# Kernel tuning notes

Measured on AMD Instinct MI355X. Metric: run time of the kernel, lower is better.

Reference implementation:

```python
import jax, jax.numpy as jnp
import numpy as np

B, HGT, WID, D, NS = 4, 64, 128, 128, 2
LN_EPS = 1e-5

def layer_norm(x, g, b):
    m = jnp.mean(x, axis=-1, keepdims=True)
    v = jnp.mean((x - m) ** 2, axis=-1, keepdims=True)
    return (x - m) * jax.lax.rsqrt(v + LN_EPS) * g + b

def setup_inputs() -> dict:
    key = jax.random.key(0)
    ks = jax.random.split(key, 8)
    src = jax.random.normal(ks[0], (B, HGT * WID, D), jnp.float32)
    L = (HGT // NS) * (WID // NS)  # 2048
    s = 0.05
    return {
        "source": src,
        "target": src,  # identical -> self-attention branch in original
        "shifted_window_attn_mask": jax.random.normal(ks[1], (NS * NS, L, L), jnp.float32),
        "shifted_window_attn_mask_1d": jnp.zeros((NS, WID // NS, WID // NS), jnp.float32),
        "height": HGT,
        "width": WID,
        "attn_num_splits": NS,
        "with_shift": 1,
        "Wq": jax.random.normal(ks[2], (D, D), jnp.float32) * s,
        "Wk": jax.random.normal(ks[3], (D, D), jnp.float32) * s,
        "Wv": jax.random.normal(ks[4], (D, D), jnp.float32) * s,
        "Wm": jax.random.normal(ks[5], (D, D), jnp.float32) * s,
        "g1": jnp.ones((D,), jnp.float32),
        "b1": jnp.zeros((D,), jnp.float32),
        "W1": jax.random.normal(ks[6], (2 * D, 8 * D), jnp.float32) * s,
        "W2": jax.random.normal(ks[7], (8 * D, D), jnp.float32) * s,
        "g2": jnp.ones((D,), jnp.float32),
        "b2": jnp.zeros((D,), jnp.float32),
    }

def _shifted_window_self_attn(q, k, v, ns, with_shift, h, w, attn_mask):
    b, _, c = q.shape
    hh, ww = h // ns, w // ns  # window sizes
    sh, sw = hh // 2, ww // 2
    L = hh * ww

    def to_windows(x):
        x = x.reshape(b, h, w, c)
        if with_shift:
            x = jnp.roll(x, shift=(-sh, -sw), axis=(1, 2))
        # (b, ns, hh, ns, ww, c) -> (b*ns*ns, hh*ww, c)
        x = x.reshape(b, ns, hh, ns, ww, c).transpose(0, 1, 3, 2, 4, 5)
        return x.reshape(b * ns * ns, L, c)

    qw, kw, vw = to_windows(q), to_windows(k), to_windows(v)
    scores = jnp.einsum("bqc,bkc->bqk", qw, kw) / (c ** 0.5)  # (b*ns^2, L, L)
    if with_shift:
        scores = (scores.reshape(b, ns * ns, L, L) + attn_mask).reshape(b * ns * ns, L, L)
    attn = jax.nn.softmax(scores, axis=-1)
    out = jnp.einsum("bqk,bkc->bqc", attn, vw)
    # merge windows back
    out = out.reshape(b, ns, ns, hh, ww, c).transpose(0, 1, 3, 2, 4, 5).reshape(b, h, w, c)
    if with_shift:
        out = jnp.roll(out, shift=(sh, sw), axis=(1, 2))
    return out.reshape(b, h * w, c)

def reference(source, target, shifted_window_attn_mask, shifted_window_attn_mask_1d,
              height, width, attn_num_splits, with_shift,
              Wq, Wk, Wv, Wm, g1, b1, W1, W2, g2, b2):
    # target == source -> self-attention, attn_num_splits > 1 -> shifted-window path
    q = source @ Wq
    k = target @ Wk
    v = target @ Wv
    message = _shifted_window_self_attn(q, k, v, attn_num_splits, with_shift,
                                        height, width, shifted_window_attn_mask)
    message = layer_norm(message @ Wm, g1, b1)
    h = jnp.concatenate([source, message], axis=-1)  # (B, HW, 2D)
    message = jax.nn.gelu(h @ W1, approximate=False) @ W2
    message = layer_norm(message, g2, b2)
    return source + message
```

## Files before the change

kernel.cpp:

```cpp
#include <hip/hip_runtime.h>

typedef unsigned short u16;
typedef __bf16 bf16x8 __attribute__((ext_vector_type(8)));
typedef float f32x4 __attribute__((ext_vector_type(4)));

#define MFMA(a, b, c) __builtin_amdgcn_mfma_f32_16x16x32_bf16(a, b, c, 0, 0, 0)


__device__ __forceinline__ u16 f2b(float f) {
  unsigned u = __builtin_bit_cast(unsigned, f);
  u += 0x7fffu + ((u >> 16) & 1u);
  return (u16)(u >> 16);
}
__device__ __forceinline__ float b2f(u16 h) {
  unsigned u = (unsigned)h << 16;
  return __builtin_bit_cast(float, u);
}
__device__ __forceinline__ void glds16(const u16* g, u16* l) {
  __builtin_amdgcn_global_load_lds((const __attribute__((address_space(1))) void*)g,
                                   (__attribute__((address_space(3))) void*)l, 16, 0, 0);
}

#define QW_OFF   ((size_t)0)
#define KW_OFF   ((size_t)8 << 20)
#define VBUF_OFF ((size_t)16 << 20)
#define O1_OFF   ((size_t)24 << 20)
#define O2_OFF   ((size_t)40 << 20)
#define SRCB_OFF ((size_t)64 << 20)
#define MSG1_OFF ((size_t)72 << 20)
#define L1_OFF   ((size_t)80 << 20)
#define L2P_OFF  (((size_t)80 << 20) + 131072)
#define WQT_OFF  (((size_t)80 << 20) + 262144)
#define WKT_OFF  (WQT_OFF + 32768)
#define WVT_OFF  (WQT_OFF + 65536)
#define WMT_OFF  (WQT_OFF + 98304)
#define W1T_OFF  (WQT_OFF + 131072)
#define W2T_OFF  (WQT_OFF + 655360)

__global__ void k_prep(const float* __restrict__ wq, const float* __restrict__ wk,
                       const float* __restrict__ wv, const float* __restrict__ wm,
                       const float* __restrict__ w1, const float* __restrict__ w2,
                       u16* __restrict__ wqt, u16* __restrict__ wkt,
                       u16* __restrict__ wvt, u16* __restrict__ wmt,
                       u16* __restrict__ w1t, u16* __restrict__ w2t) {
  int t = blockIdx.x * 256 + threadIdx.x;
  if (t < 65536) {
    int m = t >> 14, loc = t & 16383;
    int n = loc >> 7, k = loc & 127;
    const float* s = (m == 0) ? wq : (m == 1) ? wk : (m == 2) ? wv : wm;
    u16* d = (m == 0) ? wqt : (m == 1) ? wkt : (m == 2) ? wvt : wmt;
    const float sc = (m == 0) ? 0.08838834764831845f : 1.0f;
    d[n * 128 + k] = f2b(s[k * 128 + n] * sc);
  } else if (t < 65536 + 262144) {
    int loc = t - 65536;
    int n = loc >> 8, k = loc & 255;
    w1t[n * 256 + k] = f2b(w1[k * 1024 + n]);
  } else if (t < 65536 + 262144 + 131072) {
    int loc = t - 327680;
    int n = loc >> 10, k = loc & 1023;
    w2t[n * 1024 + k] = f2b(w2[k * 128 + n]);
  }
}

__global__ __launch_bounds__(256, 2)
void k_qkv(const float* __restrict__ src,
           const u16* __restrict__ wtq, const u16* __restrict__ wtk,
           const u16* __restrict__ wtv,
           u16* __restrict__ qw, u16* __restrict__ kw, u16* __restrict__ vbuf,
           u16* __restrict__ srcb) {
  __shared__ __align__(16) u16 At[64 * 136];
  __shared__ __align__(16) u16 Bt[128 * 136];
  const int tid = threadIdx.x, bid = blockIdx.x;
  const int lane = tid & 63, wid = tid >> 6;
  const int l15 = lane & 15, quad = lane >> 4;

  {
    const int row = tid >> 2, part = tid & 3;
    const int t = bid * 64 + row;
    const int g = t >> 11, p = t & 2047;
    const int b = g >> 2, wi = (g >> 1) & 1, wj = g & 1;
    const int ii = p >> 6, jj = p & 63;
    const int y = (wi * 32 + ii + 16) & 63;
    const int x = (wj * 64 + jj + 32) & 127;
    const int srow = b * 8192 + y * 128 + x;
    const float4* sp = (const float4*)(src + srow * 128) + part * 8;
    u16* lp = &At[row * 136 + part * 32];
    u16* gp = srcb + srow * 128 + part * 32;
#pragma unroll
    for (int q = 0; q < 8; ++q) {
      float4 v = sp[q];
      ushort4 h = make_ushort4(f2b(v.x), f2b(v.y), f2b(v.z), f2b(v.w));
      *(ushort4*)(lp + q * 4) = h;
      *(ushort4*)(gp + q * 4) = h;
    }
  }
  __syncthreads();

  bf16x8 afrag[4];
  const int arow = wid * 16 + l15;
#pragma unroll
  for (int kk = 0; kk < 4; ++kk)
    afrag[kk] = *(const bf16x8*)&At[arow * 136 + kk * 32 + quad * 8];

  const f32x4 fz = {0.f, 0.f, 0.f, 0.f};
#pragma unroll 1
  for (int m = 0; m < 3; ++m) {
    const u16* wp = (m == 0) ? wtq : (m == 1) ? wtk : wtv;
    {
      const int n = tid >> 1, half = tid & 1;
      const uint4* sp = (const uint4*)(wp + n * 128 + half * 64);
      uint4* dp = (uint4*)&Bt[n * 136 + half * 64];
#pragma unroll
      for (int q = 0; q < 8; ++q) dp[q] = sp[q];
    }
    __syncthreads();
    f32x4 acc[8];
#pragma unroll
    for (int nt = 0; nt < 8; ++nt) acc[nt] = fz;
#pragma unroll
    for (int kk = 0; kk < 4; ++kk) {
#pragma unroll
      for (int nt = 0; nt < 8; ++nt) {
        bf16x8 bfr = *(const bf16x8*)&Bt[(nt * 16 + l15) * 136 + kk * 32 + quad * 8];
        acc[nt] = MFMA(afrag[kk], bfr, acc[nt]);
      }
    }
    const int t0 = bid * 64 + wid * 16 + quad * 4;
    if (m < 2) {
      u16* dst = (m == 0) ? qw : kw;
#pragma unroll
      for (int nt = 0; nt < 8; ++nt) {
        const int d = nt * 16 + l15;
#pragma unroll
        for (int r = 0; r < 4; ++r) dst[(t0 + r) * 128 + d] = f2b(acc[nt][r]);
      }
    } else {
      const int g = bid >> 5;
      const int p0 = t0 & 2047;
#pragma unroll
      for (int nt = 0; nt < 8; ++nt) {
        const int d = nt * 16 + l15;
        ushort4 hv = make_ushort4(f2b(acc[nt][0]), f2b(acc[nt][1]),
                                  f2b(acc[nt][2]), f2b(acc[nt][3]));
        *(ushort4*)&vbuf[g * 262144 + d * 2048 + p0] = hv;
      }
    }
    __syncthreads();
  }
}

__global__ __launch_bounds__(256, 2)
void k_attn(const u16* __restrict__ qw, const u16* __restrict__ kw,
            const u16* __restrict__ vbuf, const float* __restrict__ mask,
            u16* __restrict__ o1, u16* __restrict__ o2,
            float* __restrict__ l1, float* __restrict__ l2) {
  __shared__ __align__(16) u16 Kt[2][64 * 128];
  __shared__ __align__(16) u16 Pt[128 * 40];
  const int tid = threadIdx.x;
  const int bid = (blockIdx.x & 7) * 64 + (blockIdx.x >> 3);
  const int lane = tid & 63, wid = tid >> 6;
  const int l15 = lane & 15, quad = lane >> 4;
  const int qb = bid & 15, half = (bid >> 4) & 1, g = bid >> 5;
  const int w = g & 3;
  const int k0 = half * 1024;
  const u16* kbase = kw + g * 262144 + k0 * 128;
  const u16* vbase = vbuf + g * 262144 + k0;
  const int qrow0 = qb * 128 + wid * 32;
  const float* mlane = mask + (size_t)w * 4194304 + (size_t)(qrow0 + quad * 4) * 2048 + k0 + l15;

  int offk[4], dstb[4];
#pragma unroll
  for (int j = 0; j < 4; ++j) {
    const int s = wid * 256 + j * 64 + lane;
    const int rk = s >> 4, bk = (s & 15) ^ (rk & 15);
    offk[j] = rk * 128 + bk * 8;
    dstb[j] = (wid * 256 + j * 64) * 8;
  }

  bf16x8 qfrag[2][4];
#pragma unroll
  for (int qs = 0; qs < 2; ++qs) {
    const u16* qp = qw + g * 262144 + (qrow0 + qs * 16 + l15) * 128 + quad * 8;
#pragma unroll
    for (int kk = 0; kk < 4; ++kk) qfrag[qs][kk] = *(const bf16x8*)(qp + kk * 32);
  }
  const f32x4 fz = {0.f, 0.f, 0.f, 0.f};
  f32x4 o[2][8];
#pragma unroll
  for (int qs = 0; qs < 2; ++qs)
#pragma unroll
    for (int nt = 0; nt < 8; ++nt) o[qs][nt] = fz;
  float lr[2][4] = {{0.f, 0.f, 0.f, 0.f}, {0.f, 0.f, 0.f, 0.f}};
  const float L2E = 1.4426950408889634f;

#pragma unroll
  for (int j = 0; j < 4; ++j) glds16(kbase + offk[j], &Kt[0][dstb[j]]);
  float mpf[16];
#pragma unroll
  for (int qs = 0; qs < 2; ++qs)
#pragma unroll
    for (int ntl = 0; ntl < 2; ++ntl)
#pragma unroll
      for (int r = 0; r < 4; ++r)
        mpf[qs * 8 + ntl * 4 + r] = mlane[(qs * 16 + r) * 2048 + ntl * 16];

#pragma unroll 1
  for (int kt = 0; kt < 16; ++kt) {
    const int p = kt & 1;
    __syncthreads();
    if (kt < 15) {
      const u16* kb = kbase + (kt + 1) * 8192;
#pragma unroll
      for (int j = 0; j < 4; ++j) glds16(kb + offk[j], &Kt[p ^ 1][dstb[j]]);
    }
#pragma unroll
    for (int ks = 0; ks < 2; ++ks) {
      bf16x8 vf[8];
      const u16* vp = vbase + kt * 64 + ks * 32 + quad * 8;
#pragma unroll
      for (int nt = 0; nt < 8; ++nt)
        vf[nt] = *(const bf16x8*)(vp + (size_t)(nt * 16 + l15) * 2048);
      float mn[16];
      const bool hasn = (kt < 15) || (ks == 0);
      const int ncol = kt * 64 + 32 + ks * 32;
      if (hasn) {
#pragma unroll
        for (int qs = 0; qs < 2; ++qs)
#pragma unroll
          for (int ntl = 0; ntl < 2; ++ntl)
#pragma unroll
            for (int r = 0; r < 4; ++r)
              mn[qs * 8 + ntl * 4 + r] = mlane[(qs * 16 + r) * 2048 + ncol + ntl * 16];
      }
      f32x4 s[2][2];
#pragma unroll
      for (int qs = 0; qs < 2; ++qs)
#pragma unroll
        for (int ntl = 0; ntl < 2; ++ntl)
#pragma unroll
          for (int r = 0; r < 4; ++r) s[qs][ntl][r] = mpf[qs * 8 + ntl * 4 + r];
#pragma unroll
      for (int kk = 0; kk < 4; ++kk)
#pragma unroll
        for (int ntl = 0; ntl < 2; ++ntl) {
          bf16x8 kfr = *(const bf16x8*)&Kt[p][(ks * 32 + ntl * 16 + l15) * 128 +
                                             (((kk * 4 + quad) ^ l15) * 8)];
          s[0][ntl] = MFMA(qfrag[0][kk], kfr, s[0][ntl]);
          s[1][ntl] = MFMA(qfrag[1][kk], kfr, s[1][ntl]);
        }
#pragma unroll
      for (int qs = 0; qs < 2; ++qs)
#pragma unroll
        for (int ntl = 0; ntl < 2; ++ntl)
#pragma unroll
          for (int r = 0; r < 4; ++r) {
            const float pv = exp2f(s[qs][ntl][r] * L2E);
            lr[qs][r] += pv;
            Pt[(wid * 32 + qs * 16 + quad * 4 + r) * 40 + ntl * 16 + l15] = f2b(pv);
          }
      bf16x8 pf0 = *(const bf16x8*)&Pt[(wid * 32 + l15) * 40 + quad * 8];
      bf16x8 pf1 = *(const bf16x8*)&Pt[(wid * 32 + 16 + l15) * 40 + quad * 8];
#pragma unroll
      for (int nt = 0; nt < 8; ++nt) {
        o[0][nt] = MFMA(pf0, vf[nt], o[0][nt]);
        o[1][nt] = MFMA(pf1, vf[nt], o[1][nt]);
      }
      if (hasn) {
#pragma unroll
        for (int i = 0; i < 16; ++i) mpf[i] = mn[i];
      }
    }
  }

#pragma unroll
  for (int off = 1; off < 16; off <<= 1)
#pragma unroll
    for (int qs = 0; qs < 2; ++qs)
#pragma unroll
      for (int r = 0; r < 4; ++r) lr[qs][r] += __shfl_xor(lr[qs][r], off, 16);
  u16* op = half ? o2 : o1;
  float* lp = half ? l2 : l1;
#pragma unroll
  for (int qs = 0; qs < 2; ++qs) {
    const int t0 = g * 2048 + qrow0 + qs * 16 + quad * 4;
#pragma unroll
    for (int r = 0; r < 4; ++r) {
      const float inv = 1.f / lr[qs][r];
#pragma unroll
      for (int nt = 0; nt < 8; ++nt)
        op[(size_t)(t0 + r) * 128 + nt * 16 + l15] = f2b(o[qs][nt][r] * inv);
      if (l15 == 0) lp[t0 + r] = lr[qs][r];
    }
  }
}

__global__ __launch_bounds__(256, 2)
void k_wmln(const u16* __restrict__ o1, const u16* __restrict__ o2,
            const float* __restrict__ l1, const float* __restrict__ l2,
            const u16* __restrict__ wmt, const float* __restrict__ g1,
            const float* __restrict__ b1, u16* __restrict__ msg1) {
  __shared__ __align__(16) u16 At[64 * 136];
  __shared__ __align__(16) u16 Bt[128 * 136];
  const int tid = threadIdx.x, bid = blockIdx.x;
  const int lane = tid & 63, wid = tid >> 6;
  const int l15 = lane & 15, quad = lane >> 4;
  {
    const int row = tid >> 2, part = tid & 3;
    const int m = bid * 64 + row;
    const float la = l1[m], lb = l2[m];
    const float wA = la / (la + lb), wB = lb / (la + lb);
    const u16* p1 = o1 + (size_t)m * 128 + part * 32;
    const u16* p2 = o2 + (size_t)m * 128 + part * 32;
    u16* lp = &At[row * 136 + part * 32];
#pragma unroll
    for (int q = 0; q < 4; ++q) {
      ushort4 xa = *(const ushort4*)(p1 + q * 8);
      ushort4 xb = *(const ushort4*)(p1 + q * 8 + 4);
      ushort4 ya = *(const ushort4*)(p2 + q * 8);
      ushort4 yb = *(const ushort4*)(p2 + q * 8 + 4);
      ushort4 ha = make_ushort4(f2b(b2f(xa.x) * wA + b2f(ya.x) * wB),
                                f2b(b2f(xa.y) * wA + b2f(ya.y) * wB),
                                f2b(b2f(xa.z) * wA + b2f(ya.z) * wB),
                                f2b(b2f(xa.w) * wA + b2f(ya.w) * wB));
      ushort4 hb = make_ushort4(f2b(b2f(xb.x) * wA + b2f(yb.x) * wB),
                                f2b(b2f(xb.y) * wA + b2f(yb.y) * wB),
                                f2b(b2f(xb.z) * wA + b2f(yb.z) * wB),
                                f2b(b2f(xb.w) * wA + b2f(yb.w) * wB));
      *(ushort4*)(lp + q * 8) = ha;
      *(ushort4*)(lp + q * 8 + 4) = hb;
    }
  }
  {
    const int n = tid >> 1, half = tid & 1;
    const uint4* sp = (const uint4*)(wmt + n * 128 + half * 64);
    uint4* dp = (uint4*)&Bt[n * 136 + half * 64];
#pragma unroll
    for (int q = 0; q < 8; ++q) dp[q] = sp[q];
  }
  __syncthreads();
  bf16x8 afrag[4];
  const int arow = wid * 16 + l15;
#pragma unroll
  for (int kk = 0; kk < 4; ++kk)
    afrag[kk] = *(const bf16x8*)&At[arow * 136 + kk * 32 + quad * 8];
  const f32x4 fz = {0.f, 0.f, 0.f, 0.f};
  f32x4 acc[8];
#pragma unroll
  for (int nt = 0; nt < 8; ++nt) acc[nt] = fz;
#pragma unroll
  for (int kk = 0; kk < 4; ++kk)
#pragma unroll
    for (int nt = 0; nt < 8; ++nt) {
      bf16x8 bfr = *(const bf16x8*)&Bt[(nt * 16 + l15) * 136 + kk * 32 + quad * 8];
      acc[nt] = MFMA(afrag[kk], bfr, acc[nt]);
    }
  float sum[4] = {0, 0, 0, 0}, sq[4] = {0, 0, 0, 0};
#pragma unroll
  for (int nt = 0; nt < 8; ++nt)
#pragma unroll
    for (int r = 0; r < 4; ++r) {
      const float v = acc[nt][r];
      sum[r] += v;
      sq[r] += v * v;
    }
#pragma unroll
  for (int off = 1; off < 16; off <<= 1)
#pragma unroll
    for (int r = 0; r < 4; ++r) {
      sum[r] += __shfl_xor(sum[r], off, 16);
      sq[r] += __shfl_xor(sq[r], off, 16);
    }
  float mean[4], rstd[4];
#pragma unroll
  for (int r = 0; r < 4; ++r) {
    mean[r] = sum[r] * (1.f / 128.f);
    const float var = sq[r] * (1.f / 128.f) - mean[r] * mean[r];
    rstd[r] = rsqrtf(var + 1e-5f);
  }
  const int t0 = bid * 64 + wid * 16 + quad * 4;
#pragma unroll
  for (int nt = 0; nt < 8; ++nt) {
    const int d = nt * 16 + l15;
    const float gg = g1[d], bb = b1[d];
#pragma unroll
    for (int r = 0; r < 4; ++r) {
      const int tt = t0 + r;
      const int gw = tt >> 11, pp = tt & 2047;
      const int bb2 = gw >> 2, wi = (gw >> 1) & 1, wj = gw & 1;
      const int ii = pp >> 6, jj = pp & 63;
      const int yy = (wi * 32 + ii + 16) & 63;
      const int xx = (wj * 64 + jj + 32) & 127;
      msg1[(bb2 * 8192 + yy * 128 + xx) * 128 + d] =
          f2b((acc[nt][r] - mean[r]) * rstd[r] * gg + bb);
    }
  }
}

__global__ __launch_bounds__(256, 2)
void k_mlp(const u16* __restrict__ srcb, const u16* __restrict__ msg1,
           const u16* __restrict__ w1t, const u16* __restrict__ w2t,
           const float* __restrict__ g2, const float* __restrict__ b2,
           const float* __restrict__ src, float* __restrict__ out) {
  __shared__ __align__(16) u16 Bt1[64 * 256];
  __shared__ __align__(16) u16 Bt2[128 * 64];
  __shared__ __align__(16) u16 Ht[64 * 72];
  const int tid = threadIdx.x, bid = blockIdx.x;
  const int lane = tid & 63, wid = tid >> 6;
  const int l15 = lane & 15, quad = lane >> 4;

  int off1[8], db1[8], off2[4], db2[4];
#pragma unroll
  for (int j = 0; j < 8; ++j) {
    const int s = wid * 512 + j * 64 + lane;
    const int r = s >> 5, c = s & 31;
    off1[j] = r * 256 + (c ^ (r & 15)) * 8;
    db1[j] = (wid * 512 + j * 64) * 8;
  }
#pragma unroll
  for (int j = 0; j < 4; ++j) {
    const int s = wid * 256 + j * 64 + lane;
    const int r = s >> 3, c = s & 7;
    off2[j] = r * 1024 + (c ^ (r & 7)) * 8;
    db2[j] = (wid * 256 + j * 64) * 8;
  }

  bf16x8 afrag[8];
  {
    const int row = bid * 64 + wid * 16 + l15;
    const u16* sp = srcb + (size_t)row * 128 + quad * 8;
    const u16* mp = msg1 + (size_t)row * 128 + quad * 8;
#pragma unroll
    for (int kk = 0; kk < 4; ++kk) {
      afrag[kk] = *(const bf16x8*)(sp + kk * 32);
      afrag[kk + 4] = *(const bf16x8*)(mp + kk * 32);
    }
  }
  const f32x4 fz = {0.f, 0.f, 0.f, 0.f};
  f32x4 oacc[8];
#pragma unroll
  for (int nt = 0; nt < 8; ++nt) oacc[nt] = fz;

#pragma unroll 1
  for (int hc = 0; hc < 16; ++hc) {
    __syncthreads();
#pragma unroll
    for (int j = 0; j < 8; ++j) glds16(w1t + hc * 16384 + off1[j], &Bt1[db1[j]]);
#pragma unroll
    for (int j = 0; j < 4; ++j) glds16(w2t + hc * 64 + off2[j], &Bt2[db2[j]]);
    __syncthreads();

    f32x4 hacc[4];
#pragma unroll
    for (int nt = 0; nt < 4; ++nt) hacc[nt] = fz;
#pragma unroll
    for (int kk = 0; kk < 8; ++kk)
#pragma unroll
      for (int nt = 0; nt < 4; ++nt) {
        bf16x8 b1 = *(const bf16x8*)&Bt1[(nt * 16 + l15) * 256 +
                                         (((kk * 4 + quad) ^ l15) * 8)];
        hacc[nt] = MFMA(afrag[kk], b1, hacc[nt]);
      }
#pragma unroll
    for (int nt = 0; nt < 4; ++nt)
#pragma unroll
      for (int r = 0; r < 4; ++r) {
        const float x = hacc[nt][r];
        const float y = 0.5f * x * (1.f + erff(x * 0.70710678118654752f));
        Ht[(wid * 16 + quad * 4 + r) * 72 + nt * 16 + l15] = f2b(y);
      }
    bf16x8 hf0 = *(const bf16x8*)&Ht[(wid * 16 + l15) * 72 + quad * 8];
    bf16x8 hf1 = *(const bf16x8*)&Ht[(wid * 16 + l15) * 72 + 32 + quad * 8];
#pragma unroll
    for (int kk2 = 0; kk2 < 2; ++kk2)
#pragma unroll
      for (int nt = 0; nt < 8; ++nt) {
        bf16x8 b2f_ = *(const bf16x8*)&Bt2[(nt * 16 + l15) * 64 +
                                           (((kk2 * 4 + quad) ^ (l15 & 7)) * 8)];
        oacc[nt] = MFMA(kk2 ? hf1 : hf0, b2f_, oacc[nt]);
      }
  }

  float sum[4] = {0, 0, 0, 0}, sq[4] = {0, 0, 0, 0};
#pragma unroll
  for (int nt = 0; nt < 8; ++nt)
#pragma unroll
    for (int r = 0; r < 4; ++r) {
      const float v = oacc[nt][r];
      sum[r] += v;
      sq[r] += v * v;
    }
#pragma unroll
  for (int off = 1; off < 16; off <<= 1)
#pragma unroll
    for (int r = 0; r < 4; ++r) {
      sum[r] += __shfl_xor(sum[r], off, 16);
      sq[r] += __shfl_xor(sq[r], off, 16);
    }
  float mean[4], rstd[4];
#pragma unroll
  for (int r = 0; r < 4; ++r) {
    mean[r] = sum[r] * (1.f / 128.f);
    const float var = sq[r] * (1.f / 128.f) - mean[r] * mean[r];
    rstd[r] = rsqrtf(var + 1e-5f);
  }
  const int t0 = bid * 64 + wid * 16 + quad * 4;
#pragma unroll
  for (int nt = 0; nt < 8; ++nt) {
    const int d = nt * 16 + l15;
    const float gg = g2[d], bb = b2[d];
#pragma unroll
    for (int r = 0; r < 4; ++r) {
      const int idx = (t0 + r) * 128 + d;
      out[idx] = src[idx] + (oacc[nt][r] - mean[r]) * rstd[r] * gg + bb;
    }
  }
}

extern "C" void kernel_launch(void* const* d_in, const int* in_sizes, int n_in,
                              void* d_out, int out_size, void* d_ws, size_t ws_size,
                              hipStream_t stream) {
  const float* src  = (const float*)d_in[0];
  const float* mask = (const float*)d_in[2];
  const float* Wq = (const float*)d_in[8];
  const float* Wk = (const float*)d_in[9];
  const float* Wv = (const float*)d_in[10];
  const float* Wm = (const float*)d_in[11];
  const float* g1 = (const float*)d_in[12];
  const float* b1 = (const float*)d_in[13];
  const float* W1 = (const float*)d_in[14];
  const float* W2 = (const float*)d_in[15];
  const float* g2 = (const float*)d_in[16];
  const float* b2 = (const float*)d_in[17];
  char* ws = (char*)d_ws;
  u16* qw   = (u16*)(ws + QW_OFF);
  u16* kw   = (u16*)(ws + KW_OFF);
  u16* vbuf = (u16*)(ws + VBUF_OFF);
  u16* o1   = (u16*)(ws + O1_OFF);
  u16* o2   = (u16*)(ws + O2_OFF);
  float* l1 = (float*)(ws + L1_OFF);
  float* l2 = (float*)(ws + L2P_OFF);
  u16* srcb = (u16*)(ws + SRCB_OFF);
  u16* msg1 = (u16*)(ws + MSG1_OFF);
  u16* wqt = (u16*)(ws + WQT_OFF);
  u16* wkt = (u16*)(ws + WKT_OFF);
  u16* wvt = (u16*)(ws + WVT_OFF);
  u16* wmt = (u16*)(ws + WMT_OFF);
  u16* w1t = (u16*)(ws + W1T_OFF);
  u16* w2t = (u16*)(ws + W2T_OFF);

  k_prep<<<1792, 256, 0, stream>>>(Wq, Wk, Wv, Wm, W1, W2, wqt, wkt, wvt, wmt, w1t, w2t);
  k_qkv<<<512, 256, 0, stream>>>(src, wqt, wkt, wvt, qw, kw, vbuf, srcb);
  k_attn<<<512, 256, 0, stream>>>(qw, kw, vbuf, mask, o1, o2, l1, l2);
  k_wmln<<<512, 256, 0, stream>>>(o1, o2, l1, l2, wmt, g1, b1, msg1);
  k_mlp<<<512, 256, 0, stream>>>(srcb, msg1, w1t, w2t, g2, b2, src, (float*)d_out);
}
```

Before: 316.6 us.

## Stage V through LDS in attention and double MLP rows per block

The attention kernel now double-buffers V tiles into LDS with async global-to-LDS loads, replacing per-lane strided global reads, and remaps block indices so blocks sharing a window mask run adjacently. The window-merge/roll scatter moves from the Wm+LN kernel's store into the MLP kernel's gather of msg1, so stores become contiguous. The MLP kernel processes 128 tokens per block instead of 64, reusing each W1/W2 LDS tile across twice as many rows with half the grid. This adds LDS and register pressure and reduces the number of blocks, which may hurt occupancy.

```diff
diff --git a/kernel.cpp b/kernel.cpp
--- a/kernel.cpp
+++ b/kernel.cpp
@@ -155,25 +155,28 @@
             u16* __restrict__ o1, u16* __restrict__ o2,
             float* __restrict__ l1, float* __restrict__ l2) {
   __shared__ __align__(16) u16 Kt[2][64 * 128];
+  __shared__ __align__(16) u16 Vt[2][128 * 64];
   __shared__ __align__(16) u16 Pt[128 * 40];
   const int tid = threadIdx.x;
   const int bid = (blockIdx.x & 7) * 64 + (blockIdx.x >> 3);
   const int lane = tid & 63, wid = tid >> 6;
   const int l15 = lane & 15, quad = lane >> 4;
-  const int qb = bid & 15, half = (bid >> 4) & 1, g = bid >> 5;
-  const int w = g & 3;
+  const int b = bid & 3, w = (bid >> 2) & 3, half = (bid >> 4) & 1, qb = bid >> 5;
+  const int g = b * 4 + w;
   const int k0 = half * 1024;
   const u16* kbase = kw + g * 262144 + k0 * 128;
   const u16* vbase = vbuf + g * 262144 + k0;
   const int qrow0 = qb * 128 + wid * 32;
   const float* mlane = mask + (size_t)w * 4194304 + (size_t)(qrow0 + quad * 4) * 2048 + k0 + l15;
 
-  int offk[4], dstb[4];
+  int offk[4], offv[4], dstb[4];
 #pragma unroll
   for (int j = 0; j < 4; ++j) {
     const int s = wid * 256 + j * 64 + lane;
     const int rk = s >> 4, bk = (s & 15) ^ (rk & 15);
     offk[j] = rk * 128 + bk * 8;
+    const int dv = s >> 3, bv = (s & 7) ^ (dv & 7);
+    offv[j] = dv * 2048 + bv * 8;
     dstb[j] = (wid * 256 + j * 64) * 8;
   }
 
@@ -194,7 +197,10 @@
   const float L2E = 1.4426950408889634f;
 
 #pragma unroll
-  for (int j = 0; j < 4; ++j) glds16(kbase + offk[j], &Kt[0][dstb[j]]);
+  for (int j = 0; j < 4; ++j) {
+    glds16(kbase + offk[j], &Kt[0][dstb[j]]);
+    glds16(vbase + offv[j], &Vt[0][dstb[j]]);
+  }
   float mpf[16];
 #pragma unroll
   for (int qs = 0; qs < 2; ++qs)
@@ -210,16 +216,15 @@
     __syncthreads();
     if (kt < 15) {
       const u16* kb = kbase + (kt + 1) * 8192;
-#pragma unroll
-      for (int j = 0; j < 4; ++j) glds16(kb + offk[j], &Kt[p ^ 1][dstb[j]]);
+      const u16* vb = vbase + (kt + 1) * 64;
+#pragma unroll
+      for (int j = 0; j < 4; ++j) {
+        glds16(kb + offk[j], &Kt[p ^ 1][dstb[j]]);
+        glds16(vb + offv[j], &Vt[p ^ 1][dstb[j]]);
+      }
     }
 #pragma unroll
     for (int ks = 0; ks < 2; ++ks) {
-      bf16x8 vf[8];
-      const u16* vp = vbase + kt * 64 + ks * 32 + quad * 8;
-#pragma unroll
-      for (int nt = 0; nt < 8; ++nt)
-        vf[nt] = *(const bf16x8*)(vp + (size_t)(nt * 16 + l15) * 2048);
       float mn[16];
       const bool hasn = (kt < 15) || (ks == 0);
       const int ncol = kt * 64 + 32 + ks * 32;
@@ -262,8 +267,10 @@
       bf16x8 pf1 = *(const bf16x8*)&Pt[(wid * 32 + 16 + l15) * 40 + quad * 8];
 #pragma unroll
       for (int nt = 0; nt < 8; ++nt) {
-        o[0][nt] = MFMA(pf0, vf[nt], o[0][nt]);
-        o[1][nt] = MFMA(pf1, vf[nt], o[1][nt]);
+        bf16x8 vfr = *(const bf16x8*)&Vt[p][(nt * 16 + l15) * 64 +
+                                            (((ks * 4 + quad) ^ (l15 & 7)) * 8)];
+        o[0][nt] = MFMA(pf0, vfr, o[0][nt]);
+        o[1][nt] = MFMA(pf1, vfr, o[1][nt]);
       }
       if (hasn) {
 #pragma unroll
@@ -385,13 +392,7 @@
 #pragma unroll
     for (int r = 0; r < 4; ++r) {
       const int tt = t0 + r;
-      const int gw = tt >> 11, pp = tt & 2047;
-      const int bb2 = gw >> 2, wi = (gw >> 1) & 1, wj = gw & 1;
-      const int ii = pp >> 6, jj = pp & 63;
-      const int yy = (wi * 32 + ii + 16) & 63;
-      const int xx = (wj * 64 + jj + 32) & 127;
-      msg1[(bb2 * 8192 + yy * 128 + xx) * 128 + d] =
-          f2b((acc[nt][r] - mean[r]) * rstd[r] * gg + bb);
+      msg1[(size_t)tt * 128 + d] = f2b((acc[nt][r] - mean[r]) * rstd[r] * gg + bb);
     }
   }
 }
@@ -403,7 +404,7 @@
            const float* __restrict__ src, float* __restrict__ out) {
   __shared__ __align__(16) u16 Bt1[64 * 256];
   __shared__ __align__(16) u16 Bt2[128 * 64];
-  __shared__ __align__(16) u16 Ht[64 * 72];
+  __shared__ __align__(16) u16 Ht[128 * 72];
   const int tid = threadIdx.x, bid = blockIdx.x;
   const int lane = tid & 63, wid = tid >> 6;
   const int l15 = lane & 15, quad = lane >> 4;
@@ -424,21 +425,28 @@
     db2[j] = (wid * 256 + j * 64) * 8;
   }
 
-  bf16x8 afrag[8];
-  {
-    const int row = bid * 64 + wid * 16 + l15;
-    const u16* sp = srcb + (size_t)row * 128 + quad * 8;
-    const u16* mp = msg1 + (size_t)row * 128 + quad * 8;
+  bf16x8 afrag[2][8];
+#pragma unroll
+  for (int qs = 0; qs < 2; ++qs) {
+    const int t_sp = bid * 128 + qs * 64 + wid * 16 + l15;
+    const u16* sp = srcb + (size_t)t_sp * 128 + quad * 8;
+    const int bb = t_sp >> 13, rem = t_sp & 8191;
+    const int y = rem >> 7, x = rem & 127;
+    const int u = (y + 48) & 63, v = (x + 96) & 127;
+    const int wrow = (bb * 4 + (u >> 5) * 2 + (v >> 6)) * 2048 + (u & 31) * 64 + (v & 63);
+    const u16* mp = msg1 + (size_t)wrow * 128 + quad * 8;
 #pragma unroll
     for (int kk = 0; kk < 4; ++kk) {
-      afrag[kk] = *(const bf16x8*)(sp + kk * 32);
-      afrag[kk + 4] = *(const bf16x8*)(mp + kk * 32);
+      afrag[qs][kk] = *(const bf16x8*)(sp + kk * 32);
+      afrag[qs][kk + 4] = *(const bf16x8*)(mp + kk * 32);
     }
   }
   const f32x4 fz = {0.f, 0.f, 0.f, 0.f};
-  f32x4 oacc[8];
-#pragma unroll
-  for (int nt = 0; nt < 8; ++nt) oacc[nt] = fz;
+  f32x4 oacc[2][8];
+#pragma unroll
+  for (int qs = 0; qs < 2; ++qs)
+#pragma unroll
+    for (int nt = 0; nt < 8; ++nt) oacc[qs][nt] = fz;
 
 #pragma unroll 1
   for (int hc = 0; hc < 16; ++hc) {
@@ -449,69 +457,82 @@
     for (int j = 0; j < 4; ++j) glds16(w2t + hc * 64 + off2[j], &Bt2[db2[j]]);
     __syncthreads();
 
-    f32x4 hacc[4];
-#pragma unroll
-    for (int nt = 0; nt < 4; ++nt) hacc[nt] = fz;
+    f32x4 hacc[2][4];
+#pragma unroll
+    for (int qs = 0; qs < 2; ++qs)
+#pragma unroll
+      for (int nt = 0; nt < 4; ++nt) hacc[qs][nt] = fz;
 #pragma unroll
     for (int kk = 0; kk < 8; ++kk)
 #pragma unroll
       for (int nt = 0; nt < 4; ++nt) {
         bf16x8 b1 = *(const bf16x8*)&Bt1[(nt * 16 + l15) * 256 +
                                          (((kk * 4 + quad) ^ l15) * 8)];
-        hacc[nt] = MFMA(afrag[kk], b1, hacc[nt]);
-      }
-#pragma unroll
-    for (int nt = 0; nt < 4; ++nt)
+        hacc[0][nt] = MFMA(afrag[0][kk], b1, hacc[0][nt]);
+        hacc[1][nt] = MFMA(afrag[1][kk], b1, hacc[1][nt]);
+      }
+#pragma unroll
+    for (int qs = 0; qs < 2; ++qs)
+#pragma unroll
+      for (int nt = 0; nt < 4; ++nt)
+#pragma unroll
+        for (int r = 0; r < 4; ++r) {
+          const float x = hacc[qs][nt][r];
+          const float y = 0.5f * x * (1.f + erff(x * 0.70710678118654752f));
+          Ht[(qs * 64 + wid * 16 + quad * 4 + r) * 72 + nt * 16 + l15] = f2b(y);
+        }
+    bf16x8 hf[2][2];
+#pragma unroll
+    for (int qs = 0; qs < 2; ++qs) {
+      hf[qs][0] = *(const bf16x8*)&Ht[(qs * 64 + wid * 16 + l15) * 72 + quad * 8];
+      hf[qs][1] = *(const bf16x8*)&Ht[(qs * 64 + wid * 16 + l15) * 72 + 32 + quad * 8];
+    }
+#pragma unroll
+    for (int kk2 = 0; kk2 < 2; ++kk2)
+#pragma unroll
+      for (int nt = 0; nt < 8; ++nt) {
+        bf16x8 b2fr = *(const bf16x8*)&Bt2[(nt * 16 + l15) * 64 +
+                                           (((kk2 * 4 + quad) ^ (l15 & 7)) * 8)];
+        oacc[0][nt] = MFMA(hf[0][kk2], b2fr, oacc[0][nt]);
+        oacc[1][nt] = MFMA(hf[1][kk2], b2fr, oacc[1][nt]);
+      }
+  }
+
+#pragma unroll
+  for (int qs = 0; qs < 2; ++qs) {
+    float sum[4] = {0, 0, 0, 0}, sq[4] = {0, 0, 0, 0};
+#pragma unroll
+    for (int nt = 0; nt < 8; ++nt)
 #pragma unroll
       for (int r = 0; r < 4; ++r) {
-        const float x = hacc[nt][r];
-        const float y = 0.5f * x * (1.f + erff(x * 0.70710678118654752f));
-        Ht[(wid * 16 + quad * 4 + r) * 72 + nt * 16 + l15] = f2b(y);
-      }
-    bf16x8 hf0 = *(const bf16x8*)&Ht[(wid * 16 + l15) * 72 + quad * 8];
-    bf16x8 hf1 = *(const bf16x8*)&Ht[(wid * 16 + l15) * 72 + 32 + quad * 8];
-#pragma unroll
-    for (int kk2 = 0; kk2 < 2; ++kk2)
-#pragma unroll
-      for (int nt = 0; nt < 8; ++nt) {
-        bf16x8 b2f_ = *(const bf16x8*)&Bt2[(nt * 16 + l15) * 64 +
-                                           (((kk2 * 4 + quad) ^ (l15 & 7)) * 8)];
-        oacc[nt] = MFMA(kk2 ? hf1 : hf0, b2f_, oacc[nt]);
-      }
-  }
-
-  float sum[4] = {0, 0, 0, 0}, sq[4] = {0, 0, 0, 0};
-#pragma unroll
-  for (int nt = 0; nt < 8; ++nt)
+        const float v = oacc[qs][nt][r];
+        sum[r] += v;
+        sq[r] += v * v;
+      }
+#pragma unroll
+    for (int off = 1; off < 16; off <<= 1)
+#pragma unroll
+      for (int r = 0; r < 4; ++r) {
+        sum[r] += __shfl_xor(sum[r], off, 16);
+        sq[r] += __shfl_xor(sq[r], off, 16);
+      }
+    float mean[4], rstd[4];
 #pragma unroll
     for (int r = 0; r < 4; ++r) {
-      const float v = oacc[nt][r];
-      sum[r] += v;
-      sq[r] += v * v;
-    }
-#pragma unroll
-  for (int off = 1; off < 16; off <<= 1)
-#pragma unroll
-    for (int r = 0; r < 4; ++r) {
-      sum[r] += __shfl_xor(sum[r], off, 16);
-      sq[r] += __shfl_xor(sq[r], off, 16);
-    }
-  float mean[4], rstd[4];
-#pragma unroll
-  for (int r = 0; r < 4; ++r) {
-    mean[r] = sum[r] * (1.f / 128.f);
-    const float var = sq[r] * (1.f / 128.f) - mean[r] * mean[r];
-    rstd[r] = rsqrtf(var + 1e-5f);
-  }
-  const int t0 = bid * 64 + wid * 16 + quad * 4;
-#pragma unroll
-  for (int nt = 0; nt < 8; ++nt) {
-    const int d = nt * 16 + l15;
-    const float gg = g2[d], bb = b2[d];
-#pragma unroll
-    for (int r = 0; r < 4; ++r) {
-      const int idx = (t0 + r) * 128 + d;
-      out[idx] = src[idx] + (oacc[nt][r] - mean[r]) * rstd[r] * gg + bb;
+      mean[r] = sum[r] * (1.f / 128.f);
+      const float var = sq[r] * (1.f / 128.f) - mean[r] * mean[r];
+      rstd[r] = rsqrtf(var + 1e-5f);
+    }
+    const int t0 = bid * 128 + qs * 64 + wid * 16 + quad * 4;
+#pragma unroll
+    for (int nt = 0; nt < 8; ++nt) {
+      const int d = nt * 16 + l15;
+      const float gg = g2[d], bb = b2[d];
+#pragma unroll
+      for (int r = 0; r < 4; ++r) {
+        const int idx = (t0 + r) * 128 + d;
+        out[idx] = src[idx] + (oacc[qs][nt][r] - mean[r]) * rstd[r] * gg + bb;
+      }
     }
   }
 }
@@ -552,5 +573,5 @@
   k_qkv<<<512, 256, 0, stream>>>(src, wqt, wkt, wvt, qw, kw, vbuf, srcb);
   k_attn<<<512, 256, 0, stream>>>(qw, kw, vbuf, mask, o1, o2, l1, l2);
   k_wmln<<<512, 256, 0, stream>>>(o1, o2, l1, l2, wmt, g1, b1, msg1);
-  k_mlp<<<512, 256, 0, stream>>>(srcb, msg1, w1t, w2t, g2, b2, src, (float*)d_out);
-}
+  k_mlp<<<256, 256, 0, stream>>>(srcb, msg1, w1t, w2t, g2, b2, src, (float*)d_out);
+}
```

Result: no change. 315.7 us (-0.3%).
